# Kernel optimization log

Hardware: AMD Instinct MI355X
Metric: run time of the kernel (lower is better)

Reference implementation:

```python
import jax, jax.numpy as jnp
import numpy as np

INF = 1000000000.0
D = 1024


def setup_inputs() -> dict:
    key = jax.random.key(0)
    k_enc, k_r = jax.random.split(key)
    encoding = jax.random.normal(k_enc, (8, 2048, D), dtype=jnp.float32)
    R = jax.random.normal(k_r, (D, D), dtype=jnp.float32) / D  # init_with_zeros=False
    return {"encoding": encoding, "R": R}


def reference(encoding, R):
    b, n, d = encoding.shape
    # Q = encoding @ R ; scores = Q @ encoding^T  (bilinear relation attention)
    encR = jnp.einsum("bnd,de->bne", encoding, R)          # [b, n, d]
    scores = jnp.einsum("bnd,bmd->bnm", encR, encoding)     # [b, n, n]
    # causal mask: -INF above the diagonal (use_mask=True)
    mask = jnp.where(jnp.tril(jnp.ones((n, n), dtype=bool)), 0.0, -INF).astype(scores.dtype)
    A = jax.nn.softmax(scores + mask, axis=2)               # [b, n, n]
    return jnp.einsum("bnm,bmd->bnd", A, encoding)          # [b, n, d]
```

## Files before the change

kernel.cpp:

```cpp
#include <hip/hip_runtime.h>
#include <hip/hip_bf16.h>


typedef __attribute__((ext_vector_type(4))) float f32x4;
typedef __attribute__((ext_vector_type(4))) unsigned u32x4;
typedef __attribute__((ext_vector_type(8))) __fp16 f16x8;
typedef __attribute__((ext_vector_type(4))) __fp16 f16x4;
typedef __attribute__((ext_vector_type(2))) __fp16 f16x2;

#define MFMA16H(A, B, C) __builtin_amdgcn_mfma_f32_16x16x32_f16(A, B, C, 0, 0, 0)

__device__ __forceinline__ f16x4 cvt4h(f32x4 a) {
    union { f16x4 v; f16x2 h[2]; } r;
    r.h[0] = __builtin_amdgcn_cvt_pkrtz(a[0], a[1]);
    r.h[1] = __builtin_amdgcn_cvt_pkrtz(a[2], a[3]);
    return r.v;
}

__device__ __forceinline__ void gload16(const void* g, void* l) {
    __builtin_amdgcn_global_load_lds(
        (const __attribute__((address_space(1))) unsigned*)g,
        (__attribute__((address_space(3))) unsigned*)l, 16, 0, 0);
}

#define BAR() do { __builtin_amdgcn_sched_barrier(0); \
                   __builtin_amdgcn_s_barrier();      \
                   __builtin_amdgcn_sched_barrier(0); } while (0)

__global__ __launch_bounds__(256) void transpose_cvt_kernel(
    const float* __restrict__ src, __fp16* __restrict__ dstT,
    __fp16* __restrict__ dstH, int R, int C)
{
    __shared__ __align__(16) char lt[64 * 128];
    const int t = threadIdx.x;
    const int bz = blockIdx.z;
    const int r0 = blockIdx.x * 64, c0 = blockIdx.y * 64;
    const size_t so = (size_t)bz * R * C;
    const int tr = t >> 4;
    const int tc4 = (t & 15) * 4;
#pragma unroll
    for (int p = 0; p < 4; ++p) {
        int rl = tr + 16 * p;
        f32x4 x = *(const f32x4*)(src + so + (size_t)(r0 + rl) * C + c0 + tc4);
        f16x4 h = cvt4h(x);
        if (dstH) *(f16x4*)(dstH + so + (size_t)(r0 + rl) * C + c0 + tc4) = h;
        *(f16x4*)(lt + rl * 128 + ((tc4 * 2) ^ ((rl & 7) << 4))) = h;
    }
    __syncthreads();
#pragma unroll
    for (int p = 0; p < 4; ++p) {
        int dl = tr + 16 * p;
#pragma unroll
        for (int j = 0; j < 4; ++j) {
            int kl = (t & 15) + 16 * j;
            __fp16 v = *(const __fp16*)(lt + kl * 128 + ((dl * 2) ^ ((kl & 7) << 4)));
            dstT[so + (size_t)(c0 + dl) * R + r0 + kl] = v;
        }
    }
}

__global__ __launch_bounds__(512, 2) void gemm_qr256(
    const __fp16* __restrict__ encH, const __fp16* __restrict__ Rt,
    __fp16* __restrict__ Qh)
{
    __shared__ __align__(16) char lds[131072];
    const int t = threadIdx.x;
    const int w = t >> 6, l = t & 63;
    const int l15 = l & 15, lg = (l >> 4) & 3;
    const int wr = w >> 2, wc = w & 3;
    const int bm = ((int)blockIdx.x >> 2) * 256;
    const int bn = ((int)blockIdx.x & 3) * 256;
    const __fp16* Ag = encH + (size_t)bm * 1024;
    const __fp16* Bg = Rt + (size_t)bn * 1024;

    const int srow = 32 * w + (l >> 2);
    const int slg = ((l & 3) - ((l >> 3) & 3)) & 3;
    const int slotr = ((l >> 4) + ((l & 15) >> 1)) & 3;

    f32x4 acc[8][4];
#pragma unroll
    for (int i = 0; i < 8; ++i)
#pragma unroll
        for (int j = 0; j < 4; ++j) acc[i][j] = (f32x4){0.f, 0.f, 0.f, 0.f};

    auto stage = [&](int op, int tile, int kh) {
        const __fp16* src = (op ? Bg : Ag) + (size_t)srow * 1024 + tile * 64 + kh * 32 + slg * 8;
        char* dst = lds + (tile & 1) * 65536 + op * 32768 + kh * 16384 + w * 2048;
        gload16(src, dst);
        gload16(src + (size_t)16 * 1024, dst + 1024);
    };
    auto rdA = [&](int buf, int ks, int mf) {
        return *(const f16x8*)(lds + buf * 65536 + ks * 16384
                               + (128 * wr + 16 * mf + l15) * 64 + slotr * 16);
    };
    auto rdB = [&](int buf, int ks, int nf) {
        return *(const f16x8*)(lds + buf * 65536 + 32768 + ks * 16384
                               + (64 * wc + 16 * nf + l15) * 64 + slotr * 16);
    };

    stage(0, 0, 0); stage(1, 0, 0); stage(0, 0, 1); stage(1, 0, 1);
    stage(0, 1, 0); stage(1, 1, 0);

    f16x8 afr[4], bfr[4];

#define MF16(mbase)                                                     \
    __builtin_amdgcn_s_setprio(1);                                      \
    _Pragma("unroll") for (int mf = 0; mf < 4; ++mf)                    \
        _Pragma("unroll") for (int nf = 0; nf < 4; ++nf)                \
            acc[(mbase) + mf][nf] = MFMA16H(afr[mf], bfr[nf], acc[(mbase) + mf][nf]); \
    __builtin_amdgcn_s_setprio(0);

    for (int i = 0; i < 8; ++i) {
        const bool lastI = (i == 7);
        asm volatile("s_waitcnt vmcnt(8)" ::: "memory");
        BAR();
#pragma unroll
        for (int nf = 0; nf < 4; ++nf) bfr[nf] = rdB(0, 0, nf);
#pragma unroll
        for (int mf = 0; mf < 4; ++mf) afr[mf] = rdA(0, 0, mf);
        stage(0, 2 * i + 1, 1);
        MF16(0)
        BAR();
#pragma unroll
        for (int mf = 0; mf < 4; ++mf) afr[mf] = rdA(0, 0, mf + 4);
        stage(1, 2 * i + 1, 1);
        MF16(4)
        asm volatile("s_waitcnt vmcnt(8)" ::: "memory");
        BAR();
#pragma unroll
        for (int nf = 0; nf < 4; ++nf) bfr[nf] = rdB(0, 1, nf);
#pragma unroll
        for (int mf = 0; mf < 4; ++mf) afr[mf] = rdA(0, 1, mf);
        if (!lastI) stage(0, 2 * i + 2, 0);
        MF16(0)
        BAR();
#pragma unroll
        for (int mf = 0; mf < 4; ++mf) afr[mf] = rdA(0, 1, mf + 4);
        if (!lastI) stage(1, 2 * i + 2, 0);
        MF16(4)
        if (!lastI) asm volatile("s_waitcnt vmcnt(8)" ::: "memory");
        else        asm volatile("s_waitcnt vmcnt(4)" ::: "memory");
        BAR();
#pragma unroll
        for (int nf = 0; nf < 4; ++nf) bfr[nf] = rdB(1, 0, nf);
#pragma unroll
        for (int mf = 0; mf < 4; ++mf) afr[mf] = rdA(1, 0, mf);
        if (!lastI) stage(0, 2 * i + 2, 1);
        MF16(0)
        BAR();
#pragma unroll
        for (int mf = 0; mf < 4; ++mf) afr[mf] = rdA(1, 0, mf + 4);
        if (!lastI) stage(1, 2 * i + 2, 1);
        MF16(4)
        if (!lastI) asm volatile("s_waitcnt vmcnt(8)" ::: "memory");
        else        asm volatile("s_waitcnt vmcnt(0)" ::: "memory");
        BAR();
#pragma unroll
        for (int nf = 0; nf < 4; ++nf) bfr[nf] = rdB(1, 1, nf);
#pragma unroll
        for (int mf = 0; mf < 4; ++mf) afr[mf] = rdA(1, 1, mf);
        if (!lastI) stage(0, 2 * i + 3, 0);
        MF16(0)
        BAR();
#pragma unroll
        for (int mf = 0; mf < 4; ++mf) afr[mf] = rdA(1, 1, mf + 4);
        if (!lastI) stage(1, 2 * i + 3, 0);
        MF16(4)
    }
#undef MF16

#pragma unroll
    for (int mf = 0; mf < 8; ++mf)
#pragma unroll
        for (int nf = 0; nf < 4; ++nf)
#pragma unroll
            for (int rg = 0; rg < 4; ++rg) {
                int rr = bm + 128 * wr + 16 * mf + 4 * lg + rg;
                int cc = bn + 64 * wc + 16 * nf + l15;
                Qh[(size_t)rr * 1024 + cc] = (__fp16)acc[mf][nf][rg];
            }
}

template <int CMODE>
__device__ __forceinline__ void core256x128(
    const __fp16* __restrict__ A, int ldA, const __fp16* __restrict__ B, int ldB,
    char* __restrict__ Cptr, int ldC, int K, int rowOff, int colOff, bool maskDiag)
{
    __shared__ __align__(16) char lds[98304];
    const int t = threadIdx.x;
    const int w = t >> 6, l = t & 63;
    const int l15 = l & 15, lg = (l >> 4) & 3;
    const int wr = w >> 1, wc = w & 1;

    const int srowA = 32 * w + (l >> 2);
    const int srowB = 16 * w + (l >> 2);
    const int slg = ((l & 3) - ((l >> 3) & 3)) & 3;
    const int slotr = ((l >> 4) + ((l & 15) >> 1)) & 3;

    f32x4 acc[4][4];
#pragma unroll
    for (int i = 0; i < 4; ++i)
#pragma unroll
        for (int j = 0; j < 4; ++j) acc[i][j] = (f32x4){0.f, 0.f, 0.f, 0.f};

    auto stageA = [&](int tile, int kh) {
        const __fp16* src = A + (size_t)srowA * ldA + tile * 64 + kh * 32 + slg * 8;
        char* dst = lds + (tile & 1) * 49152 + kh * 16384 + w * 2048;
        gload16(src, dst);
        gload16(src + (size_t)16 * ldA, dst + 1024);
    };
    auto stageB = [&](int tile, int kh) {
        const __fp16* src = B + (size_t)srowB * ldB + tile * 64 + kh * 32 + slg * 8;
        char* dst = lds + (tile & 1) * 49152 + 32768 + kh * 8192 + w * 1024;
        gload16(src, dst);
    };
    auto rdA = [&](int buf, int kh, int mf) {
        return *(const f16x8*)(lds + buf * 49152 + kh * 16384
                               + (64 * wr + 16 * mf + l15) * 64 + slotr * 16);
    };
    auto rdB = [&](int buf, int kh, int nf) {
        return *(const f16x8*)(lds + buf * 49152 + 32768 + kh * 8192
                               + (64 * wc + 16 * nf + l15) * 64 + slotr * 16);
    };

    stageA(0, 0); stageB(0, 0);
    stageA(0, 1); stageB(0, 1);
    stageA(1, 0); stageB(1, 0);

    f16x8 afr[4], bfr[4];
    const int nIter = K >> 7;

#define MFPH()                                                          \
    __builtin_amdgcn_s_setprio(1);                                      \
    _Pragma("unroll") for (int mf = 0; mf < 4; ++mf)                    \
        _Pragma("unroll") for (int nf = 0; nf < 4; ++nf)                \
            acc[mf][nf] = MFMA16H(afr[mf], bfr[nf], acc[mf][nf]);       \
    __builtin_amdgcn_s_setprio(0);

    for (int i = 0; i < nIter; ++i) {
        const bool lastI = (i == nIter - 1);
        asm volatile("s_waitcnt vmcnt(6)" ::: "memory");
        BAR();
#pragma unroll
        for (int nf = 0; nf < 4; ++nf) bfr[nf] = rdB(0, 0, nf);
#pragma unroll
        for (int mf = 0; mf < 4; ++mf) afr[mf] = rdA(0, 0, mf);
        stageA(2 * i + 1, 1); stageB(2 * i + 1, 1);
        MFPH()
        asm volatile("s_waitcnt vmcnt(6)" ::: "memory");
        BAR();
#pragma unroll
        for (int nf = 0; nf < 4; ++nf) bfr[nf] = rdB(0, 1, nf);
#pragma unroll
        for (int mf = 0; mf < 4; ++mf) afr[mf] = rdA(0, 1, mf);
        if (!lastI) { stageA(2 * i + 2, 0); stageB(2 * i + 2, 0); }
        MFPH()
        if (!lastI) asm volatile("s_waitcnt vmcnt(6)" ::: "memory");
        else        asm volatile("s_waitcnt vmcnt(3)" ::: "memory");
        BAR();
#pragma unroll
        for (int nf = 0; nf < 4; ++nf) bfr[nf] = rdB(1, 0, nf);
#pragma unroll
        for (int mf = 0; mf < 4; ++mf) afr[mf] = rdA(1, 0, mf);
        if (!lastI) { stageA(2 * i + 2, 1); stageB(2 * i + 2, 1); }
        MFPH()
        if (!lastI) asm volatile("s_waitcnt vmcnt(6)" ::: "memory");
        else        asm volatile("s_waitcnt vmcnt(0)" ::: "memory");
        BAR();
#pragma unroll
        for (int nf = 0; nf < 4; ++nf) bfr[nf] = rdB(1, 1, nf);
#pragma unroll
        for (int mf = 0; mf < 4; ++mf) afr[mf] = rdA(1, 1, mf);
        if (!lastI) { stageA(2 * i + 3, 0); stageB(2 * i + 3, 0); }
        MFPH()
    }
#undef MFPH
    BAR();

#pragma unroll
    for (int mf = 0; mf < 4; ++mf)
#pragma unroll
        for (int nf = 0; nf < 4; ++nf)
#pragma unroll
            for (int rg = 0; rg < 4; ++rg) {
                int rr = 64 * wr + 16 * mf + 4 * lg + rg;
                int cc = 64 * wc + 16 * nf + l15;
                float v = acc[mf][nf][rg];
                if (CMODE == 2) {
                    *(float*)(Cptr + ((size_t)rr * ldC + cc) * 4) = v;
                } else {
                    if (maskDiag && colOff + cc > rowOff + rr) v = -30000.f;
                    *(__fp16*)(Cptr + ((size_t)rr * ldC + cc) * 2) = (__fp16)v;
                }
            }
}

__global__ __launch_bounds__(512, 2) void gemm_s256(
    const __fp16* __restrict__ Qh, const __fp16* __restrict__ encH,
    __fp16* __restrict__ S)
{
    const int b = (int)blockIdx.x & 7;
    const int r = (int)blockIdx.x >> 3;
    int qt = 0;
    while (r >= (qt + 1) * (qt + 2)) ++qt;
    const int nt = r - qt * (qt + 1);
    const size_t bo = (size_t)b * 2048 * 1024;
    const size_t so = (size_t)b * 2048 * 2048;
    core256x128<1>(Qh + bo + (size_t)(256 * qt) * 1024, 1024,
                   encH + bo + (size_t)(128 * nt) * 1024, 1024,
                   (char*)(S + so + (size_t)(256 * qt) * 2048 + 128 * nt), 2048,
                   1024, 256 * qt, 128 * nt, (nt >> 1) == qt);
}

__global__ __launch_bounds__(512, 2) void gemm_pv256(
    const __fp16* __restrict__ P, const __fp16* __restrict__ encT,
    float* __restrict__ out)
{
    const int b = (int)blockIdx.x & 7;
    const int r = (int)blockIdx.x >> 3;
    const int a = r >> 3, dblk = r & 7;
    const size_t so = (size_t)b * 2048 * 2048;
    const size_t to = (size_t)b * 1024 * 2048;
    const size_t oo = (size_t)b * 2048 * 1024;
#pragma unroll
    for (int pass = 0; pass < 2; ++pass) {
        const int qtb = pass ? 7 - a : a;
        core256x128<2>(P + so + (size_t)(256 * qtb) * 2048, 2048,
                       encT + to + (size_t)(128 * dblk) * 2048, 2048,
                       (char*)(out + oo + (size_t)(256 * qtb) * 1024 + 128 * dblk), 1024,
                       256 * (qtb + 1), 0, 0, false);
    }
}

__global__ __launch_bounds__(256) void softmax_kernel(__fp16* __restrict__ S, int sh)
{
    const int t = threadIdx.x;
    const int wv = t >> 6, l = t & 63;
    const int r = blockIdx.x * 4 + wv;
    const int b = blockIdx.y;
    __fp16* row = S + ((size_t)b * 2048 + r) * 2048;
    const int L = ((r >> sh) + 1) << sh;

    float v[4][8];
    float mx = -1e30f;
#pragma unroll
    for (int i = 0; i < 4; ++i) {
        int c0 = 8 * l + 512 * i;
        if (c0 < L) {
            f16x8 h = *reinterpret_cast<const f16x8*>(row + c0);
#pragma unroll
            for (int j = 0; j < 8; ++j) { v[i][j] = (float)h[j]; mx = fmaxf(mx, v[i][j]); }
        } else {
#pragma unroll
            for (int j = 0; j < 8; ++j) v[i][j] = -1e30f;
        }
    }
#pragma unroll
    for (int off = 1; off < 64; off <<= 1) mx = fmaxf(mx, __shfl_xor(mx, off));
    float sm = 0.f;
#pragma unroll
    for (int i = 0; i < 4; ++i)
#pragma unroll
        for (int j = 0; j < 8; ++j) { v[i][j] = __expf(v[i][j] - mx); sm += v[i][j]; }
#pragma unroll
    for (int off = 1; off < 64; off <<= 1) sm += __shfl_xor(sm, off);
    const float inv = 1.f / sm;
#pragma unroll
    for (int i = 0; i < 4; ++i) {
        int c0 = 8 * l + 512 * i;
        if (c0 < L) {
            union { f16x8 v8; f16x2 h[4]; } o;
#pragma unroll
            for (int j = 0; j < 4; ++j)
                o.h[j] = __builtin_amdgcn_cvt_pkrtz(v[i][2 * j] * inv, v[i][2 * j + 1] * inv);
            *reinterpret_cast<f16x8*>(row + c0) = o.v8;
        }
    }
}

__global__ __launch_bounds__(256) void qr_gemm_kernel(
    const float* __restrict__ A, const float* __restrict__ B, float* C)
{
    __shared__ __align__(16) char sA[128 * 64];
    __shared__ __align__(16) char sB[128 * 64];
    const int t = threadIdx.x;
    const int w = t >> 6, l = t & 63;
    const int l15 = l & 15, lg = l >> 4;
    const int bm = blockIdx.x * 128;
    const int bn = blockIdx.y * 128;

    f32x4 acc[4][4];
#pragma unroll
    for (int i = 0; i < 4; ++i)
#pragma unroll
        for (int j = 0; j < 4; ++j) acc[i][j] = (f32x4){0.f, 0.f, 0.f, 0.f};

    const int kq = 4 * (t & 7);
    const int i2 = t >> 3;

    for (int kk = 0; kk < 1024; kk += 32) {
#pragma unroll
        for (int it = 0; it < 4; ++it) {
            int m = i2 + 32 * it;
            f32x4 x = *reinterpret_cast<const f32x4*>(&A[(size_t)(bm + m) * 1024 + kk + kq]);
            *reinterpret_cast<f16x4*>(sA + m * 64 + ((2 * kq) ^ (((m >> 1) & 3) << 4))) = cvt4h(x);
        }
        {
            int n0 = 4 * i2;
            f32x4 x[4];
#pragma unroll
            for (int r = 0; r < 4; ++r)
                x[r] = *reinterpret_cast<const f32x4*>(&B[(size_t)(kk + kq + r) * 1024 + bn + n0]);
#pragma unroll
            for (int j = 0; j < 4; ++j) {
                int n = n0 + j;
                union { f16x4 v; f16x2 h[2]; } s;
                s.h[0] = __builtin_amdgcn_cvt_pkrtz(x[0][j], x[1][j]);
                s.h[1] = __builtin_amdgcn_cvt_pkrtz(x[2][j], x[3][j]);
                *reinterpret_cast<f16x4*>(sB + n * 64 + ((2 * kq) ^ (((n >> 1) & 3) << 4))) = s.v;
            }
        }
        __syncthreads();
        f16x8 af[4], bfv[4];
        const int r0 = (w >> 1) * 64, c0 = (w & 1) * 64;
#pragma unroll
        for (int mt = 0; mt < 4; ++mt) {
            int m = r0 + 16 * mt + l15;
            af[mt] = *reinterpret_cast<f16x8*>(sA + m * 64 + ((16 * lg) ^ (((m >> 1) & 3) << 4)));
        }
#pragma unroll
        for (int nt = 0; nt < 4; ++nt) {
            int n = c0 + 16 * nt + l15;
            bfv[nt] = *reinterpret_cast<f16x8*>(sB + n * 64 + ((16 * lg) ^ (((n >> 1) & 3) << 4)));
        }
#pragma unroll
        for (int mt = 0; mt < 4; ++mt)
#pragma unroll
            for (int nt = 0; nt < 4; ++nt)
                acc[mt][nt] = MFMA16H(af[mt], bfv[nt], acc[mt][nt]);
        __syncthreads();
    }
#pragma unroll
    for (int mt = 0; mt < 4; ++mt)
#pragma unroll
        for (int nt = 0; nt < 4; ++nt)
#pragma unroll
            for (int rg = 0; rg < 4; ++rg) {
                int row = bm + (w >> 1) * 64 + 16 * mt + 4 * lg + rg;
                int col = bn + (w & 1) * 64 + 16 * nt + l15;
                C[(size_t)row * 1024 + col] = acc[mt][nt][rg];
            }
}

__global__ __launch_bounds__(256) void s_gemm_kernel(
    const float* __restrict__ Q, const float* __restrict__ enc, __fp16* __restrict__ S)
{
    __shared__ __align__(16) char sA[128 * 64];
    __shared__ __align__(16) char sB[128 * 64];
    const int t = threadIdx.x;
    const int w = t >> 6, l = t & 63;
    const int l15 = l & 15, lg = l >> 4;

    int rem = 135 - (int)blockIdx.x;
    int qt = 0;
    while (rem > qt) { rem -= qt + 1; ++qt; }
    const int kt = rem;
    const int b = blockIdx.y;
    const float* Arow = Q + ((size_t)b * 2048 + qt * 128) * 1024;
    const float* Brow = enc + ((size_t)b * 2048 + kt * 128) * 1024;

    f32x4 acc[4][4];
#pragma unroll
    for (int i = 0; i < 4; ++i)
#pragma unroll
        for (int j = 0; j < 4; ++j) acc[i][j] = (f32x4){0.f, 0.f, 0.f, 0.f};

    const int kq = 4 * (t & 7);
    const int i2 = t >> 3;

    for (int kk = 0; kk < 1024; kk += 32) {
#pragma unroll
        for (int it = 0; it < 4; ++it) {
            int m = i2 + 32 * it;
            int sw = (2 * kq) ^ (((m >> 1) & 3) << 4);
            f32x4 xa = *reinterpret_cast<const f32x4*>(&Arow[(size_t)m * 1024 + kk + kq]);
            f32x4 xb = *reinterpret_cast<const f32x4*>(&Brow[(size_t)m * 1024 + kk + kq]);
            *reinterpret_cast<f16x4*>(sA + m * 64 + sw) = cvt4h(xa);
            *reinterpret_cast<f16x4*>(sB + m * 64 + sw) = cvt4h(xb);
        }
        __syncthreads();
        f16x8 af[4], bfv[4];
        const int r0 = (w >> 1) * 64, c0 = (w & 1) * 64;
#pragma unroll
        for (int mt = 0; mt < 4; ++mt) {
            int m = r0 + 16 * mt + l15;
            af[mt] = *reinterpret_cast<f16x8*>(sA + m * 64 + ((16 * lg) ^ (((m >> 1) & 3) << 4)));
        }
#pragma unroll
        for (int nt = 0; nt < 4; ++nt) {
            int n = c0 + 16 * nt + l15;
            bfv[nt] = *reinterpret_cast<f16x8*>(sB + n * 64 + ((16 * lg) ^ (((n >> 1) & 3) << 4)));
        }
#pragma unroll
        for (int mt = 0; mt < 4; ++mt)
#pragma unroll
            for (int nt = 0; nt < 4; ++nt)
                acc[mt][nt] = MFMA16H(af[mt], bfv[nt], acc[mt][nt]);
        __syncthreads();
    }
    const int r0 = (w >> 1) * 64, c0 = (w & 1) * 64;
#pragma unroll
    for (int mt = 0; mt < 4; ++mt)
#pragma unroll
        for (int nt = 0; nt < 4; ++nt)
#pragma unroll
            for (int rg = 0; rg < 4; ++rg) {
                int rt = r0 + 16 * mt + 4 * lg + rg;
                int ct = c0 + 16 * nt + l15;
                float v = acc[mt][nt][rg];
                if (kt == qt && ct > rt) v = -30000.f;
                S[((size_t)b * 2048 + qt * 128 + rt) * 2048 + kt * 128 + ct] = (__fp16)v;
            }
}

__global__ __launch_bounds__(512) void pv_gemm_kernel(
    const __fp16* __restrict__ P, const float* __restrict__ enc, float* __restrict__ out)
{
    __shared__ __align__(16) char sA[128 * 128];
    __shared__ __align__(16) char sB[128 * 128];
    const int t = threadIdx.x;
    const int w = t >> 6, l = t & 63;
    const int l15 = l & 15, lg = (l >> 4) & 3;
    const int wq = w >> 2, wdv = w & 3;
    const int qtb = 15 - (int)blockIdx.x;
    const int dblk = blockIdx.y;
    const int b = blockIdx.z;
    const int q0 = 128 * qtb;
    const int nkv = 128 * (qtb + 1);
    const __fp16* Pbase = P + ((size_t)b * 2048 + q0) * 2048;
    const float* Eb = enc + (size_t)b * 2048 * 1024;

    f32x4 acc[4][2];
#pragma unroll
    for (int i = 0; i < 4; ++i)
#pragma unroll
        for (int j = 0; j < 2; ++j) acc[i][j] = (f32x4){0.f, 0.f, 0.f, 0.f};

    const int ar = t >> 2, aseg = t & 3;
    const int ba = t >> 5, bdq = t & 31;

    for (int kv0 = 0; kv0 < nkv; kv0 += 64) {
        __syncthreads();
        {
            const __fp16* src = Pbase + (size_t)ar * 2048 + kv0 + 16 * aseg;
            u32x4 v0 = *reinterpret_cast<const u32x4*>(src);
            u32x4 v1 = *reinterpret_cast<const u32x4*>(src + 8);
            const int sw = (ar & 7) << 4;
            *reinterpret_cast<u32x4*>(sA + ar * 128 + ((32 * aseg) ^ sw)) = v0;
            *reinterpret_cast<u32x4*>(sA + ar * 128 + ((32 * aseg + 16) ^ sw)) = v1;
        }
        {
            const float* src = Eb + (size_t)(kv0 + 4 * ba) * 1024 + 128 * dblk + 4 * bdq;
            f32x4 x0 = *reinterpret_cast<const f32x4*>(src);
            f32x4 x1 = *reinterpret_cast<const f32x4*>(src + 1024);
            f32x4 x2 = *reinterpret_cast<const f32x4*>(src + 2048);
            f32x4 x3 = *reinterpret_cast<const f32x4*>(src + 3072);
#pragma unroll
            for (int j = 0; j < 4; ++j) {
                int d = 4 * bdq + j;
                union { f16x4 v; f16x2 h[2]; } s;
                s.h[0] = __builtin_amdgcn_cvt_pkrtz(x0[j], x1[j]);
                s.h[1] = __builtin_amdgcn_cvt_pkrtz(x2[j], x3[j]);
                *reinterpret_cast<f16x4*>(sB + d * 128 + ((8 * ba) ^ ((d & 7) << 4))) = s.v;
            }
        }
        __syncthreads();
#pragma unroll
        for (int ks = 0; ks < 2; ++ks) {
            f16x8 afr[4], bfr[2];
#pragma unroll
            for (int mt = 0; mt < 4; ++mt) {
                int rr = 64 * wq + 16 * mt + l15;
                afr[mt] = *reinterpret_cast<f16x8*>(sA + rr * 128 + ((64 * ks + 16 * lg) ^ ((rr & 7) << 4)));
            }
#pragma unroll
            for (int nt = 0; nt < 2; ++nt) {
                int d = 32 * wdv + 16 * nt + l15;
                bfr[nt] = *reinterpret_cast<f16x8*>(sB + d * 128 + ((64 * ks + 16 * lg) ^ ((d & 7) << 4)));
            }
#pragma unroll
            for (int mt = 0; mt < 4; ++mt)
#pragma unroll
                for (int nt = 0; nt < 2; ++nt)
                    acc[mt][nt] = MFMA16H(afr[mt], bfr[nt], acc[mt][nt]);
        }
    }
#pragma unroll
    for (int mt = 0; mt < 4; ++mt)
#pragma unroll
        for (int nt = 0; nt < 2; ++nt)
#pragma unroll
            for (int rg = 0; rg < 4; ++rg) {
                size_t row = (size_t)b * 2048 + q0 + 64 * wq + 16 * mt + 4 * lg + rg;
                int col = 128 * dblk + 32 * wdv + 16 * nt + l15;
                out[row * 1024 + col] = acc[mt][nt][rg];
            }
}

extern "C" void kernel_launch(void* const* d_in, const int* in_sizes, int n_in,
                              void* d_out, int out_size, void* d_ws, size_t ws_size,
                              hipStream_t stream)
{
    const float* enc = (const float*)d_in[0];
    const float* R = (const float*)d_in[1];
    float* out = (float*)d_out;
    const size_t MB = 1u << 20;

    if (ws_size >= 98 * MB) {
        __fp16* S = (__fp16*)d_ws;
        __fp16* encT = (__fp16*)((char*)d_ws + 64 * MB);
        __fp16* Rt = (__fp16*)((char*)d_ws + 96 * MB);
        __fp16* Qh = (__fp16*)d_out;
        __fp16* encH = (__fp16*)d_out + (size_t)16384 * 1024;

        transpose_cvt_kernel<<<dim3(32, 16, 8), 256, 0, stream>>>(enc, encT, encH, 2048, 1024);
        transpose_cvt_kernel<<<dim3(16, 16, 1), 256, 0, stream>>>(R, Rt, (__fp16*)nullptr, 1024, 1024);
        gemm_qr256<<<dim3(256), 512, 0, stream>>>(encH, Rt, Qh);
        gemm_s256<<<dim3(576), 512, 0, stream>>>(Qh, encH, S);
        softmax_kernel<<<dim3(512, 8), 256, 0, stream>>>(S, 8);
        gemm_pv256<<<dim3(256), 512, 0, stream>>>(S, encT, out);
    } else {
        __fp16* S = (__fp16*)d_ws;
        qr_gemm_kernel<<<dim3(128, 8), 256, 0, stream>>>(enc, R, out);
        s_gemm_kernel<<<dim3(136, 8), 256, 0, stream>>>(out, enc, S);
        softmax_kernel<<<dim3(512, 8), 256, 0, stream>>>(S, 7);
        pv_gemm_kernel<<<dim3(16, 8, 8), 512, 0, stream>>>(S, enc, out);
    }
}
```

Measured before the change: 177.8 us.

## Use three-stage ring buffer in GEMM core, raise occupancy, split PV blocks

The shared GEMM core drops the two-buffer, four-phase K loop and uses a three-slot ring of 32-wide K slices, one barrier per slice. This cuts LDS from 96KB to 72KB per block. The S and PV GEMM kernels now request 4 blocks per CU in their launch bounds, which can push the compiler toward fewer registers or spills. The PV kernel no longer pairs two causal tiles per block; it launches twice as many blocks, each doing one query tile, with the heaviest tiles scheduled first, and relies on the hardware scheduler for load balance.

```diff
diff --git a/kernel.cpp b/kernel.cpp
--- a/kernel.cpp
+++ b/kernel.cpp
@@ -186,7 +186,7 @@
     const __fp16* __restrict__ A, int ldA, const __fp16* __restrict__ B, int ldB,
     char* __restrict__ Cptr, int ldC, int K, int rowOff, int colOff, bool maskDiag)
 {
-    __shared__ __align__(16) char lds[98304];
+    __shared__ __align__(16) char lds[73728];
     const int t = threadIdx.x;
     const int w = t >> 6, l = t & 63;
     const int l15 = l & 15, lg = (l >> 4) & 3;
@@ -203,78 +203,45 @@
 #pragma unroll
         for (int j = 0; j < 4; ++j) acc[i][j] = (f32x4){0.f, 0.f, 0.f, 0.f};
 
-    auto stageA = [&](int tile, int kh) {
-        const __fp16* src = A + (size_t)srowA * ldA + tile * 64 + kh * 32 + slg * 8;
-        char* dst = lds + (tile & 1) * 49152 + kh * 16384 + w * 2048;
-        gload16(src, dst);
-        gload16(src + (size_t)16 * ldA, dst + 1024);
+    auto stageH = [&](int h) {
+        const int reg = h % 3;
+        const __fp16* sa = A + (size_t)srowA * ldA + h * 32 + slg * 8;
+        char* da = lds + reg * 16384 + w * 2048;
+        gload16(sa, da);
+        gload16(sa + (size_t)16 * ldA, da + 1024);
+        const __fp16* sb = B + (size_t)srowB * ldB + h * 32 + slg * 8;
+        gload16(sb, lds + 49152 + reg * 8192 + w * 1024);
     };
-    auto stageB = [&](int tile, int kh) {
-        const __fp16* src = B + (size_t)srowB * ldB + tile * 64 + kh * 32 + slg * 8;
-        char* dst = lds + (tile & 1) * 49152 + 32768 + kh * 8192 + w * 1024;
-        gload16(src, dst);
-    };
-    auto rdA = [&](int buf, int kh, int mf) {
-        return *(const f16x8*)(lds + buf * 49152 + kh * 16384
+    auto rdA = [&](int h, int mf) {
+        return *(const f16x8*)(lds + (h % 3) * 16384
                                + (64 * wr + 16 * mf + l15) * 64 + slotr * 16);
     };
-    auto rdB = [&](int buf, int kh, int nf) {
-        return *(const f16x8*)(lds + buf * 49152 + 32768 + kh * 8192
+    auto rdB = [&](int h, int nf) {
+        return *(const f16x8*)(lds + 49152 + (h % 3) * 8192
                                + (64 * wc + 16 * nf + l15) * 64 + slotr * 16);
     };
 
-    stageA(0, 0); stageB(0, 0);
-    stageA(0, 1); stageB(0, 1);
-    stageA(1, 0); stageB(1, 0);
+    const int nh = K >> 5;
+    stageH(0); stageH(1);
 
     f16x8 afr[4], bfr[4];
-    const int nIter = K >> 7;
-
-#define MFPH()                                                          \
-    __builtin_amdgcn_s_setprio(1);                                      \
-    _Pragma("unroll") for (int mf = 0; mf < 4; ++mf)                    \
-        _Pragma("unroll") for (int nf = 0; nf < 4; ++nf)                \
-            acc[mf][nf] = MFMA16H(afr[mf], bfr[nf], acc[mf][nf]);       \
-    __builtin_amdgcn_s_setprio(0);
-
-    for (int i = 0; i < nIter; ++i) {
-        const bool lastI = (i == nIter - 1);
-        asm volatile("s_waitcnt vmcnt(6)" ::: "memory");
-        BAR();
-#pragma unroll
-        for (int nf = 0; nf < 4; ++nf) bfr[nf] = rdB(0, 0, nf);
-#pragma unroll
-        for (int mf = 0; mf < 4; ++mf) afr[mf] = rdA(0, 0, mf);
-        stageA(2 * i + 1, 1); stageB(2 * i + 1, 1);
-        MFPH()
-        asm volatile("s_waitcnt vmcnt(6)" ::: "memory");
-        BAR();
-#pragma unroll
-        for (int nf = 0; nf < 4; ++nf) bfr[nf] = rdB(0, 1, nf);
-#pragma unroll
-        for (int mf = 0; mf < 4; ++mf) afr[mf] = rdA(0, 1, mf);
-        if (!lastI) { stageA(2 * i + 2, 0); stageB(2 * i + 2, 0); }
-        MFPH()
-        if (!lastI) asm volatile("s_waitcnt vmcnt(6)" ::: "memory");
-        else        asm volatile("s_waitcnt vmcnt(3)" ::: "memory");
-        BAR();
-#pragma unroll
-        for (int nf = 0; nf < 4; ++nf) bfr[nf] = rdB(1, 0, nf);
-#pragma unroll
-        for (int mf = 0; mf < 4; ++mf) afr[mf] = rdA(1, 0, mf);
-        if (!lastI) { stageA(2 * i + 2, 1); stageB(2 * i + 2, 1); }
-        MFPH()
-        if (!lastI) asm volatile("s_waitcnt vmcnt(6)" ::: "memory");
-        else        asm volatile("s_waitcnt vmcnt(0)" ::: "memory");
-        BAR();
-#pragma unroll
-        for (int nf = 0; nf < 4; ++nf) bfr[nf] = rdB(1, 1, nf);
-#pragma unroll
-        for (int mf = 0; mf < 4; ++mf) afr[mf] = rdA(1, 1, mf);
-        if (!lastI) { stageA(2 * i + 3, 0); stageB(2 * i + 3, 0); }
-        MFPH()
-    }
-#undef MFPH
+    for (int h = 0; h < nh; ++h) {
+        if (h + 1 < nh) asm volatile("s_waitcnt vmcnt(3)" ::: "memory");
+        else            asm volatile("s_waitcnt vmcnt(0)" ::: "memory");
+        BAR();
+#pragma unroll
+        for (int nf = 0; nf < 4; ++nf) bfr[nf] = rdB(h, nf);
+#pragma unroll
+        for (int mf = 0; mf < 4; ++mf) afr[mf] = rdA(h, mf);
+        if (h + 2 < nh) stageH(h + 2);
+        __builtin_amdgcn_s_setprio(1);
+#pragma unroll
+        for (int mf = 0; mf < 4; ++mf)
+#pragma unroll
+            for (int nf = 0; nf < 4; ++nf)
+                acc[mf][nf] = MFMA16H(afr[mf], bfr[nf], acc[mf][nf]);
+        __builtin_amdgcn_s_setprio(0);
+    }
     BAR();
 
 #pragma unroll
@@ -295,7 +262,7 @@
             }
 }
 
-__global__ __launch_bounds__(512, 2) void gemm_s256(
+__global__ __launch_bounds__(512, 4) void gemm_s256(
     const __fp16* __restrict__ Qh, const __fp16* __restrict__ encH,
     __fp16* __restrict__ S)
 {
@@ -312,24 +279,21 @@
                    1024, 256 * qt, 128 * nt, (nt >> 1) == qt);
 }
 
-__global__ __launch_bounds__(512, 2) void gemm_pv256(
+__global__ __launch_bounds__(512, 4) void gemm_pv256(
     const __fp16* __restrict__ P, const __fp16* __restrict__ encT,
     float* __restrict__ out)
 {
     const int b = (int)blockIdx.x & 7;
     const int r = (int)blockIdx.x >> 3;
-    const int a = r >> 3, dblk = r & 7;
+    const int qtb = 7 - (r >> 3);
+    const int dblk = r & 7;
     const size_t so = (size_t)b * 2048 * 2048;
     const size_t to = (size_t)b * 1024 * 2048;
     const size_t oo = (size_t)b * 2048 * 1024;
-#pragma unroll
-    for (int pass = 0; pass < 2; ++pass) {
-        const int qtb = pass ? 7 - a : a;
-        core256x128<2>(P + so + (size_t)(256 * qtb) * 2048, 2048,
-                       encT + to + (size_t)(128 * dblk) * 2048, 2048,
-                       (char*)(out + oo + (size_t)(256 * qtb) * 1024 + 128 * dblk), 1024,
-                       256 * (qtb + 1), 0, 0, false);
-    }
+    core256x128<2>(P + so + (size_t)(256 * qtb) * 2048, 2048,
+                   encT + to + (size_t)(128 * dblk) * 2048, 2048,
+                   (char*)(out + oo + (size_t)(256 * qtb) * 1024 + 128 * dblk), 1024,
+                   256 * (qtb + 1), 0, 0, false);
 }
 
 __global__ __launch_bounds__(256) void softmax_kernel(__fp16* __restrict__ S, int sh)
@@ -628,7 +592,7 @@
         gemm_qr256<<<dim3(256), 512, 0, stream>>>(encH, Rt, Qh);
         gemm_s256<<<dim3(576), 512, 0, stream>>>(Qh, encH, S);
         softmax_kernel<<<dim3(512, 8), 256, 0, stream>>>(S, 8);
-        gemm_pv256<<<dim3(256), 512, 0, stream>>>(S, encT, out);
+        gemm_pv256<<<dim3(512), 512, 0, stream>>>(S, encT, out);
     } else {
         __fp16* S = (__fp16*)d_ws;
         qr_gemm_kernel<<<dim3(128, 8), 256, 0, stream>>>(enc, R, out);
```

Result: no change. 179.4 us (+0.9%).
